# Optimization experiments

Measured on AMD Instinct MI355X. Metric: run time of the kernel, lower is better.

## Reference

```python
import jax, jax.numpy as jnp
import numpy as np

THRESHOLD_FRAC = 0.1  # default `threshold` kwarg in RingLoss.forward


def _l2_normalize(x):
    # matches torch.nn.functional.normalize(x, p=2, dim=1, eps=1e-12)
    n = jnp.linalg.norm(x, axis=1, keepdims=True)
    return x / jnp.maximum(n, 1e-12)


def setup_inputs() -> dict:
    key = jax.random.key(0)
    k1, k2, k3 = jax.random.split(key, 3)
    N, D = 4096, 512
    h1 = jax.random.normal(k1, (N, D), dtype=jnp.float32)
    h2 = jax.random.normal(k2, (N, D), dtype=jnp.float32)
    y = jax.random.randint(k3, (N,), 0, 100)  # class labels
    tau = jnp.asarray(0.5, dtype=jnp.float32)  # contrastive temperature
    return {"h1": h1, "h2": h2, "y": y, "tau": tau}


def reference(h1, h2, y, tau):
    # NOTE: in the original module, `y` is only used to build false_neg_mask /
    # false_neg_cnt, which are dead values (never used in the returned loss).
    # The loss itself depends only on h1, h2, tau, threshold.
    N = h1.shape[0]
    t = int(N * THRESHOLD_FRAC)  # static ring cutoff

    h1n = _l2_normalize(h1)
    h2n = _l2_normalize(h2)

    s12 = h1n @ h2n.T  # [N, N] cross-view similarity
    s11 = h1n @ h1n.T  # [N, N]
    s22 = h2n @ h2n.T  # [N, N]

    neg1 = jnp.concatenate([s11, s12], axis=1)    # [N, 2N]
    neg2 = jnp.concatenate([s12.T, s22], axis=1)  # [N, 2N]

    # sort descending per row, keep the middle "ring" [t : 2N - t]
    neg1 = jnp.sort(neg1, axis=1)[:, ::-1][:, t:2 * N - t]
    neg2 = jnp.sort(neg2, axis=1)[:, ::-1][:, t:2 * N - t]

    f = lambda x: jnp.exp(x / tau)
    pos = f(jnp.diagonal(s12))      # [N]
    n1 = f(neg1).sum(axis=1)        # [N]
    n2 = f(neg2).sum(axis=1)        # [N]

    loss = 0.5 * (-jnp.log(pos / n1) - jnp.log(pos / n2))
    return loss.mean()
```

## Files before the change

kernel.cpp:

```cpp
#include <hip/hip_runtime.h>


typedef unsigned short u16;
typedef __bf16 bf16x8 __attribute__((ext_vector_type(8)));
typedef float f32x4 __attribute__((ext_vector_type(4)));
typedef u16 u16x8 __attribute__((ext_vector_type(8)));

#define NROW 8192
#define NHALF 4096
#define DIM 512
#define RING_T 409
#define NB 1024

__device__ inline u16 f2bf(float f) {
  unsigned u = __builtin_bit_cast(unsigned, f);
  unsigned r = (u + 0x7fffu + ((u >> 16) & 1u)) >> 16;
  return (u16)r;
}
__device__ inline float bf2f(u16 h) {
  unsigned u = ((unsigned)h) << 16;
  return __builtin_bit_cast(float, u);
}

__device__ inline float block_sum(float x, volatile float* s4, int t) {
  #pragma unroll
  for (int off = 32; off > 0; off >>= 1) x += __shfl_down(x, off);
  __syncthreads();
  if ((t & 63) == 0) s4[t >> 6] = x;
  __syncthreads();
  return s4[0] + s4[1] + s4[2] + s4[3];
}

__global__ __launch_bounds__(256) void normalize_k(const float* __restrict__ h1,
                                                   const float* __restrict__ h2,
                                                   u16* __restrict__ G) {
  const int r = blockIdx.x;
  const int t = threadIdx.x;
  const float* src = (r < NHALF) ? (h1 + (size_t)r * DIM) : (h2 + (size_t)(r - NHALF) * DIM);
  float2 x = *(const float2*)(src + (t << 1));
  __shared__ float s4[4];
  float tot = block_sum(x.x * x.x + x.y * x.y, s4, t);
  float scale = 1.0f / fmaxf(sqrtf(tot), 1e-12f);
  unsigned pk = (unsigned)f2bf(x.x * scale) | ((unsigned)f2bf(x.y * scale) << 16);
  *(unsigned*)(G + (size_t)r * DIM + (t << 1)) = pk;
}

__global__ __launch_bounds__(256) void diag_k(const float* __restrict__ h1,
                                              const float* __restrict__ h2,
                                              float* __restrict__ accums) {
  const int i = blockIdx.x, t = threadIdx.x;
  float2 a = *(const float2*)(h1 + (size_t)i * DIM + (t << 1));
  float2 b = *(const float2*)(h2 + (size_t)i * DIM + (t << 1));
  __shared__ float s4[4];
  float S11 = block_sum(a.x * a.x + a.y * a.y, s4, t);
  float S22 = block_sum(b.x * b.x + b.y * b.y, s4, t);
  float S12 = block_sum(a.x * b.x + a.y * b.y, s4, t);
  if (t == 0) {
    float d = S12 / (fmaxf(sqrtf(S11), 1e-12f) * fmaxf(sqrtf(S22), 1e-12f));
    atomicAdd(&accums[1], d);
  }
}

#define BK 32
#define LDK 40

__global__ __launch_bounds__(256) void gram_gemm(const u16* __restrict__ G,
                                                 u16* __restrict__ S,
                                                 int row0) {
  __shared__ u16 As[128 * LDK];
  __shared__ u16 Bs[128 * LDK];
  const int t = threadIdx.x;
  const int lane = t & 63;
  const int wave = t >> 6;
  const int wm = wave >> 1, wn = wave & 1;
  const int brow = row0 + (blockIdx.y << 7), bcol = blockIdx.x << 7;
  const int fr = lane & 15, fg = lane >> 4;

  f32x4 acc[4][4] = {};

  for (int ks = 0; ks < DIM; ks += BK) {
    u16x8 ua[2], ub[2];
    #pragma unroll
    for (int q = 0; q < 2; ++q) {
      int cid = (q << 8) + t;
      int r = cid >> 2;
      int c = ((cid & 3) + r) & 3;
      const int go = ks + c * 8;
      ua[q] = *(const u16x8*)(G + (size_t)(brow + r) * DIM + go);
      ub[q] = *(const u16x8*)(G + (size_t)(bcol + r) * DIM + go);
    }
    __syncthreads();
    #pragma unroll
    for (int q = 0; q < 2; ++q) {
      int cid = (q << 8) + t;
      int r = cid >> 2;
      int c = ((cid & 3) + r) & 3;
      *(u16x8*)(&As[r * LDK + c * 8]) = ua[q];
      *(u16x8*)(&Bs[r * LDK + c * 8]) = ub[q];
    }
    __syncthreads();

    bf16x8 af[4], bfr[4];
    #pragma unroll
    for (int m = 0; m < 4; ++m)
      af[m] = __builtin_bit_cast(bf16x8,
          *(const u16x8*)(&As[((wm << 6) + (m << 4) + fr) * LDK + (fg << 3)]));
    #pragma unroll
    for (int n = 0; n < 4; ++n)
      bfr[n] = __builtin_bit_cast(bf16x8,
          *(const u16x8*)(&Bs[((wn << 6) + (n << 4) + fr) * LDK + (fg << 3)]));
    #pragma unroll
    for (int m = 0; m < 4; ++m)
      #pragma unroll
      for (int n = 0; n < 4; ++n)
        acc[m][n] = __builtin_amdgcn_mfma_f32_16x16x32_bf16(af[m], bfr[n], acc[m][n], 0, 0, 0);
  }

  #pragma unroll
  for (int m = 0; m < 4; ++m)
    #pragma unroll
    for (int n = 0; n < 4; ++n) {
      int lrow = (blockIdx.y << 7) + (wm << 6) + (m << 4) + (fg << 2);
      int col = bcol + (wn << 6) + (n << 4) + fr;
      #pragma unroll
      for (int j = 0; j < 4; ++j)
        S[(size_t)(lrow + j) * NROW + col] = f2bf(acc[m][n][j]);
    }
}

__global__ __launch_bounds__(256) void ring_k(const u16* __restrict__ S,
                                              const float* __restrict__ taup,
                                              float* __restrict__ accums) {
  __shared__ unsigned cnt[NB];
  __shared__ unsigned sfx[NB];
  __shared__ float s4[4];
  __shared__ int bhi_s, blo_s;
  const int r = blockIdx.x, t = threadIdx.x;
  const float inv_tau = 1.0f / taup[0];

  #pragma unroll
  for (int k = 0; k < 4; ++k) cnt[t + (k << 8)] = 0;
  __syncthreads();

  float v[32];
  const u16* row = S + (size_t)r * NROW;
  #pragma unroll
  for (int q = 0; q < 4; ++q) {
    u16x8 u = *(const u16x8*)(row + (((q << 8) + t) << 3));
    #pragma unroll
    for (int j = 0; j < 8; ++j) v[(q << 3) + j] = bf2f(u[j]);
  }
  #pragma unroll
  for (int i = 0; i < 32; ++i) {
    int b = (int)((v[i] + 1.05f) * 487.61905f);
    b = b < 0 ? 0 : (b > (NB - 1) ? (NB - 1) : b);
    atomicAdd(&cnt[b], 1u);
  }
  __syncthreads();

  #pragma unroll
  for (int k = 0; k < 4; ++k) sfx[t + (k << 8)] = cnt[t + (k << 8)];
  __syncthreads();
  for (int off = 1; off < NB; off <<= 1) {
    unsigned tmp[4];
    #pragma unroll
    for (int k = 0; k < 4; ++k) {
      int i = t + (k << 8);
      tmp[k] = sfx[i] + ((i + off < NB) ? sfx[i + off] : 0u);
    }
    __syncthreads();
    #pragma unroll
    for (int k = 0; k < 4; ++k) sfx[t + (k << 8)] = tmp[k];
    __syncthreads();
  }

  #pragma unroll
  for (int k = 0; k < 4; ++k) {
    int i = t + (k << 8);
    unsigned ai = sfx[i];
    unsigned ae = (i + 1 < NB) ? sfx[i + 1] : 0u;
    if (ai >= RING_T && ae < RING_T) bhi_s = i;
    unsigned beq = NROW - ae;
    unsigned blt = NROW - ai;
    if (beq >= RING_T && blt < RING_T) blo_s = i;
  }
  __syncthreads();
  const int bh = bhi_s, bl = blo_s;

  float eTot = 0, eAb = 0, eHi = 0, eBe = 0, eLo = 0;
  #pragma unroll
  for (int i = 0; i < 32; ++i) {
    float e = __expf(v[i] * inv_tau);
    int b = (int)((v[i] + 1.05f) * 487.61905f);
    b = b < 0 ? 0 : (b > (NB - 1) ? (NB - 1) : b);
    eTot += e;
    if (b > bh) eAb += e;
    else if (b == bh) eHi += e;
    if (b < bl) eBe += e;
    else if (b == bl) eLo += e;
  }
  eTot = block_sum(eTot, s4, t);
  eAb  = block_sum(eAb, s4, t);
  eHi  = block_sum(eHi, s4, t);
  eBe  = block_sum(eBe, s4, t);
  eLo  = block_sum(eLo, s4, t);

  if (t == 0) {
    unsigned cAb = (bh + 1 < NB) ? sfx[bh + 1] : 0u;
    unsigned cBe = NROW - sfx[bl];
    unsigned ch = cnt[bh], cl = cnt[bl];
    float sumTop = eAb + (ch ? (float)(RING_T - cAb) * (eHi / (float)ch) : 0.0f);
    float sumBot = eBe + (cl ? (float)(RING_T - cBe) * (eLo / (float)cl) : 0.0f);
    float n = eTot - sumTop - sumBot;
    atomicAdd(&accums[0], 0.5f * logf(n));
  }
}

__global__ void init_k(float* accums) {
  if (threadIdx.x < 2) accums[threadIdx.x] = 0.0f;
}

__global__ void final_k(const float* __restrict__ accums,
                        const float* __restrict__ taup,
                        float* __restrict__ out) {
  out[0] = (accums[0] - accums[1] / taup[0]) * (1.0f / (float)NHALF);
}

extern "C" void kernel_launch(void* const* d_in, const int* in_sizes, int n_in,
                              void* d_out, int out_size, void* d_ws, size_t ws_size,
                              hipStream_t stream) {
  const float* h1 = (const float*)d_in[0];
  const float* h2 = (const float*)d_in[1];
  const float* taup = (const float*)d_in[3];
  float* out = (float*)d_out;

  char* ws = (char*)d_ws;
  u16* G = (u16*)ws;
  float* accums = (float*)(ws + (size_t)8 * 1024 * 1024);
  u16* Schunk = (u16*)(ws + (size_t)8 * 1024 * 1024 + 256);

  size_t avail = (ws_size > (size_t)8 * 1024 * 1024 + 256)
                     ? ws_size - (size_t)8 * 1024 * 1024 - 256 : 0;
  long long rpc = (long long)(avail / ((size_t)NROW * 2));
  rpc = (rpc / 128) * 128;
  if (rpc < 128) rpc = 128;
  if (rpc > NROW) rpc = NROW;

  hipLaunchKernelGGL(init_k, dim3(1), dim3(64), 0, stream, accums);
  hipLaunchKernelGGL(normalize_k, dim3(NROW), dim3(256), 0, stream, h1, h2, G);
  hipLaunchKernelGGL(diag_k, dim3(NHALF), dim3(256), 0, stream, h1, h2, accums);

  for (int r0 = 0; r0 < NROW; r0 += (int)rpc) {
    int rows = (int)((r0 + rpc <= NROW) ? rpc : (NROW - r0));
    hipLaunchKernelGGL(gram_gemm, dim3(64, rows >> 7), dim3(256), 0, stream,
                       G, Schunk, r0);
    hipLaunchKernelGGL(ring_k, dim3(rows), dim3(256), 0, stream,
                       Schunk, taup, accums);
  }

  hipLaunchKernelGGL(final_k, dim3(1), dim3(1), 0, stream, accums, taup, out);
}
```

Baseline: 346.5 us.

## Use direct global-to-LDS loads in GEMM and streamline ring histogram scan

The Gram GEMM now stages A/B tiles with global_load_lds straight into unpadded shared memory, skipping the trip through registers. The ring kernel moves to 256 coarser histogram buckets with one private histogram per wave, swaps the shared-memory Hillis-Steele scan for a wave-shuffle suffix scan, and merges the five block reductions into one. The aim is to cut register pressure, LDS traffic and barrier counts. In exchange, the unpadded LDS layout may cause bank conflicts on fragment reads, and coarser buckets make the interpolation of the boundary buckets in the ring approximation less exact.

Measured after the change: 333.2 us. 3.8% less time.

```diff
diff --git a/kernel.cpp b/kernel.cpp
--- a/kernel.cpp
+++ b/kernel.cpp
@@ -10,7 +10,8 @@
 #define NHALF 4096
 #define DIM 512
 #define RING_T 409
-#define NB 1024
+#define NB 256
+#define BSCALE 121.904762f
 
 __device__ inline u16 f2bf(float f) {
   unsigned u = __builtin_bit_cast(unsigned, f);
@@ -20,6 +21,10 @@
 __device__ inline float bf2f(u16 h) {
   unsigned u = ((unsigned)h) << 16;
   return __builtin_bit_cast(float, u);
+}
+__device__ inline int bucket_of(float v) {
+  int b = (int)((v + 1.05f) * BSCALE);
+  return b < 0 ? 0 : (b > (NB - 1) ? (NB - 1) : b);
 }
 
 __device__ inline float block_sum(float x, volatile float* s4, int t) {
@@ -62,13 +67,18 @@
 }
 
 #define BK 32
-#define LDK 40
+
+__device__ inline void gload_lds16(const u16* g, u16* lds_base) {
+  __builtin_amdgcn_global_load_lds(
+      (const __attribute__((address_space(1))) void*)g,
+      (__attribute__((address_space(3))) void*)lds_base, 16, 0, 0);
+}
 
 __global__ __launch_bounds__(256) void gram_gemm(const u16* __restrict__ G,
                                                  u16* __restrict__ S,
                                                  int row0) {
-  __shared__ u16 As[128 * LDK];
-  __shared__ u16 Bs[128 * LDK];
+  __shared__ u16 As[128 * BK];
+  __shared__ u16 Bs[128 * BK];
   const int t = threadIdx.x;
   const int lane = t & 63;
   const int wave = t >> 6;
@@ -76,39 +86,29 @@
   const int brow = row0 + (blockIdx.y << 7), bcol = blockIdx.x << 7;
   const int fr = lane & 15, fg = lane >> 4;
 
+  const int srow = lane >> 2;
+  const int scol = (lane & 3) << 3;
+  const int chA0 = wave, chA1 = wave + 4;
+
   f32x4 acc[4][4] = {};
 
   for (int ks = 0; ks < DIM; ks += BK) {
-    u16x8 ua[2], ub[2];
-    #pragma unroll
-    for (int q = 0; q < 2; ++q) {
-      int cid = (q << 8) + t;
-      int r = cid >> 2;
-      int c = ((cid & 3) + r) & 3;
-      const int go = ks + c * 8;
-      ua[q] = *(const u16x8*)(G + (size_t)(brow + r) * DIM + go);
-      ub[q] = *(const u16x8*)(G + (size_t)(bcol + r) * DIM + go);
-    }
     __syncthreads();
-    #pragma unroll
-    for (int q = 0; q < 2; ++q) {
-      int cid = (q << 8) + t;
-      int r = cid >> 2;
-      int c = ((cid & 3) + r) & 3;
-      *(u16x8*)(&As[r * LDK + c * 8]) = ua[q];
-      *(u16x8*)(&Bs[r * LDK + c * 8]) = ub[q];
-    }
+    gload_lds16(G + (size_t)(brow + (chA0 << 4) + srow) * DIM + ks + scol, As + (chA0 << 9));
+    gload_lds16(G + (size_t)(brow + (chA1 << 4) + srow) * DIM + ks + scol, As + (chA1 << 9));
+    gload_lds16(G + (size_t)(bcol + (chA0 << 4) + srow) * DIM + ks + scol, Bs + (chA0 << 9));
+    gload_lds16(G + (size_t)(bcol + (chA1 << 4) + srow) * DIM + ks + scol, Bs + (chA1 << 9));
     __syncthreads();
 
     bf16x8 af[4], bfr[4];
     #pragma unroll
     for (int m = 0; m < 4; ++m)
       af[m] = __builtin_bit_cast(bf16x8,
-          *(const u16x8*)(&As[((wm << 6) + (m << 4) + fr) * LDK + (fg << 3)]));
+          *(const u16x8*)(&As[(((wm << 6) + (m << 4) + fr) << 5) + (fg << 3)]));
     #pragma unroll
     for (int n = 0; n < 4; ++n)
       bfr[n] = __builtin_bit_cast(bf16x8,
-          *(const u16x8*)(&Bs[((wn << 6) + (n << 4) + fr) * LDK + (fg << 3)]));
+          *(const u16x8*)(&Bs[(((wn << 6) + (n << 4) + fr) << 5) + (fg << 3)]));
     #pragma unroll
     for (int m = 0; m < 4; ++m)
       #pragma unroll
@@ -131,15 +131,18 @@
 __global__ __launch_bounds__(256) void ring_k(const u16* __restrict__ S,
                                               const float* __restrict__ taup,
                                               float* __restrict__ accums) {
+  __shared__ unsigned hist4[4 * NB];
   __shared__ unsigned cnt[NB];
   __shared__ unsigned sfx[NB];
-  __shared__ float s4[4];
-  __shared__ int bhi_s, blo_s;
+  __shared__ unsigned wavetot[4];
+  __shared__ float red[4 * 8];
+  __shared__ int bhl[2];
   const int r = blockIdx.x, t = threadIdx.x;
+  const int lane = t & 63, w = t >> 6;
   const float inv_tau = 1.0f / taup[0];
 
   #pragma unroll
-  for (int k = 0; k < 4; ++k) cnt[t + (k << 8)] = 0;
+  for (int k = 0; k < 4; ++k) hist4[t + (k << 8)] = 0;
   __syncthreads();
 
   float v[32];
@@ -150,68 +153,71 @@
     #pragma unroll
     for (int j = 0; j < 8; ++j) v[(q << 3) + j] = bf2f(u[j]);
   }
-  #pragma unroll
-  for (int i = 0; i < 32; ++i) {
-    int b = (int)((v[i] + 1.05f) * 487.61905f);
-    b = b < 0 ? 0 : (b > (NB - 1) ? (NB - 1) : b);
-    atomicAdd(&cnt[b], 1u);
-  }
-  __syncthreads();
-
-  #pragma unroll
-  for (int k = 0; k < 4; ++k) sfx[t + (k << 8)] = cnt[t + (k << 8)];
-  __syncthreads();
-  for (int off = 1; off < NB; off <<= 1) {
-    unsigned tmp[4];
-    #pragma unroll
-    for (int k = 0; k < 4; ++k) {
-      int i = t + (k << 8);
-      tmp[k] = sfx[i] + ((i + off < NB) ? sfx[i + off] : 0u);
-    }
-    __syncthreads();
-    #pragma unroll
-    for (int k = 0; k < 4; ++k) sfx[t + (k << 8)] = tmp[k];
-    __syncthreads();
-  }
-
-  #pragma unroll
-  for (int k = 0; k < 4; ++k) {
-    int i = t + (k << 8);
-    unsigned ai = sfx[i];
-    unsigned ae = (i + 1 < NB) ? sfx[i + 1] : 0u;
-    if (ai >= RING_T && ae < RING_T) bhi_s = i;
+  unsigned* myhist = &hist4[w << 8];
+  #pragma unroll
+  for (int i = 0; i < 32; ++i) atomicAdd(&myhist[bucket_of(v[i])], 1u);
+  __syncthreads();
+
+  unsigned c = hist4[t] + hist4[t + 256] + hist4[t + 512] + hist4[t + 768];
+  cnt[t] = c;
+  unsigned x = c;
+  #pragma unroll
+  for (int off = 1; off < 64; off <<= 1) {
+    unsigned y = __shfl_down(x, off);
+    if (lane + off < 64) x += y;
+  }
+  unsigned wt = __shfl(x, 0);
+  if (lane == 0) wavetot[w] = wt;
+  __syncthreads();
+  unsigned hi = 0;
+  #pragma unroll
+  for (int k = 0; k < 4; ++k) hi += (k > w) ? wavetot[k] : 0u;
+  sfx[t] = x + hi;
+  __syncthreads();
+
+  {
+    unsigned ai = sfx[t];
+    unsigned ae = (t < NB - 1) ? sfx[t + 1] : 0u;
+    if (ai >= RING_T && ae < RING_T) bhl[0] = t;
     unsigned beq = NROW - ae;
     unsigned blt = NROW - ai;
-    if (beq >= RING_T && blt < RING_T) blo_s = i;
-  }
-  __syncthreads();
-  const int bh = bhi_s, bl = blo_s;
+    if (beq >= RING_T && blt < RING_T) bhl[1] = t;
+  }
+  __syncthreads();
+  const int bh = bhl[0], bl = bhl[1];
 
   float eTot = 0, eAb = 0, eHi = 0, eBe = 0, eLo = 0;
   #pragma unroll
   for (int i = 0; i < 32; ++i) {
     float e = __expf(v[i] * inv_tau);
-    int b = (int)((v[i] + 1.05f) * 487.61905f);
-    b = b < 0 ? 0 : (b > (NB - 1) ? (NB - 1) : b);
+    int b = bucket_of(v[i]);
     eTot += e;
-    if (b > bh) eAb += e;
-    else if (b == bh) eHi += e;
-    if (b < bl) eBe += e;
-    else if (b == bl) eLo += e;
-  }
-  eTot = block_sum(eTot, s4, t);
-  eAb  = block_sum(eAb, s4, t);
-  eHi  = block_sum(eHi, s4, t);
-  eBe  = block_sum(eBe, s4, t);
-  eLo  = block_sum(eLo, s4, t);
+    eAb += (b > bh) ? e : 0.0f;
+    eHi += (b == bh) ? e : 0.0f;
+    eBe += (b < bl) ? e : 0.0f;
+    eLo += (b == bl) ? e : 0.0f;
+  }
+  float acc5[5] = {eTot, eAb, eHi, eBe, eLo};
+  #pragma unroll
+  for (int q = 0; q < 5; ++q)
+    #pragma unroll
+    for (int off = 32; off > 0; off >>= 1) acc5[q] += __shfl_down(acc5[q], off);
+  if (lane == 0)
+    #pragma unroll
+    for (int q = 0; q < 5; ++q) red[(w << 3) + q] = acc5[q];
+  __syncthreads();
 
   if (t == 0) {
+    float s5[5];
+    #pragma unroll
+    for (int q = 0; q < 5; ++q)
+      s5[q] = red[q] + red[8 + q] + red[16 + q] + red[24 + q];
     unsigned cAb = (bh + 1 < NB) ? sfx[bh + 1] : 0u;
     unsigned cBe = NROW - sfx[bl];
     unsigned ch = cnt[bh], cl = cnt[bl];
-    float sumTop = eAb + (ch ? (float)(RING_T - cAb) * (eHi / (float)ch) : 0.0f);
-    float sumBot = eBe + (cl ? (float)(RING_T - cBe) * (eLo / (float)cl) : 0.0f);
-    float n = eTot - sumTop - sumBot;
+    float sumTop = s5[1] + (ch ? (float)(RING_T - cAb) * (s5[2] / (float)ch) : 0.0f);
+    float sumBot = s5[3] + (cl ? (float)(RING_T - cBe) * (s5[4] / (float)cl) : 0.0f);
+    float n = s5[0] - sumTop - sumBot;
     atomicAdd(&accums[0], 0.5f * logf(n));
   }
 }
```
